# Optimization experiments

Hardware: AMD Instinct MI355X
Metric: run time of the kernel (lower is better)

Reference implementation:

```python
import math
import jax
import jax.numpy as jnp
import numpy as np

MUL = 32            # multiplicity of 0e and 1o in irreps_in/out
N_NODES = 50000
N_EDGES = 800000
N_BASIS = 10
N_HID = 100
NUM_NEIGHBORS = 16.0


def setup_inputs() -> dict:
    key = jax.random.key(0)
    ks = jax.random.split(key, 14)
    return {
        "node_input": jax.random.normal(ks[0], (N_NODES, 4 * MUL), jnp.float32),
        "node_attr": jnp.ones((N_NODES, 1), jnp.float32),
        "edge_src": jax.random.randint(ks[1], (N_EDGES,), 0, N_NODES, dtype=jnp.int32),
        "edge_dst": jax.random.randint(ks[2], (N_EDGES,), 0, N_NODES, dtype=jnp.int32),
        "edge_attr": jax.random.normal(ks[3], (N_EDGES, 4), jnp.float32),
        "edge_length_embedded": jax.random.uniform(ks[4], (N_EDGES, N_BASIS), dtype=jnp.float32),
        "W_sc0": jax.random.normal(ks[5], (MUL, MUL), jnp.float32),
        "W_sc1": jax.random.normal(ks[6], (MUL, MUL), jnp.float32),
        "W_l10": jax.random.normal(ks[7], (MUL, MUL), jnp.float32),
        "W_l11": jax.random.normal(ks[8], (MUL, MUL), jnp.float32),
        "W_l20": jax.random.normal(ks[9], (2 * MUL, MUL), jnp.float32),
        "W_l21": jax.random.normal(ks[10], (2 * MUL, MUL), jnp.float32),
        "W_fc1": jax.random.normal(ks[11], (N_BASIS, N_HID), jnp.float32),
        "W_fc2": jax.random.normal(ks[12], (N_HID, 4 * MUL), jnp.float32),
    }


def _fctp(x0, x1, attr, W0, W1):
    """FullyConnectedTensorProduct with a 1x0e attr: per-irrep linear * scalar attr.
    x0: [N,U], x1: [N,U,3], attr: [N,1]. Path norm alpha = 1/sqrt(fan_in)."""
    inv = 1.0 / math.sqrt(W0.shape[0])
    o0 = attr * (x0 @ W0) * inv                                    # [N,W]
    o1 = attr[:, :, None] * jnp.einsum("nud,uw->nwd", x1, W1) * inv  # [N,W,3]
    return o0, o1


def _forward(node_input, node_attr, edge_attr, edge_length_embedded,
             W_sc0, W_sc1, W_l10, W_l11, W_l20, W_l21, W_fc1, W_fc2,
             edge_src, edge_dst):
    N = node_input.shape[0]
    x0 = node_input[:, :MUL]                       # [N,32]  0e
    x1 = node_input[:, MUL:].reshape(N, MUL, 3)    # [N,32,3] 1o

    # self-connection and lin1 (both attr is scalar 0e)
    s0, s1 = _fctp(x0, x1, node_attr, W_sc0, W_sc1)
    y0, y1 = _fctp(x0, x1, node_attr, W_l10, W_l11)

    # radial MLP -> per-edge uvu weights (weight_numel = 4*MUL)
    h = jax.nn.silu(edge_length_embedded @ W_fc1 * (1.0 / math.sqrt(N_BASIS)))
    w = h @ W_fc2 * (1.0 / math.sqrt(N_HID))       # [E,128]
    w1, w2, w3, w4 = (w[:, 0*MUL:1*MUL], w[:, 1*MUL:2*MUL],
                      w[:, 2*MUL:3*MUL], w[:, 3*MUL:4*MUL])

    # gather source node features per edge
    x0s = y0[edge_src]                              # [E,32]
    x1s = y1[edge_src]                              # [E,32,3]
    ea0 = edge_attr[:, :1]                          # [E,1]   0e
    ea1 = edge_attr[:, 1:]                          # [E,3]   1o

    # segmented uvu tensor product (CG for lmax=1, component norm)
    mid0a = w1 * x0s * ea0                                         # 0e x 0e -> 0e
    mid0b = w4 * jnp.einsum("eum,em->eu", x1s, ea1) * (1.0 / math.sqrt(3.0))  # 1o x 1o -> 0e
    mid1a = (w2 * x0s)[:, :, None] * ea1[:, None, :]               # 0e x 1o -> 1o
    mid1b = w3[:, :, None] * x1s * ea0[:, None, :]                 # 1o x 0e -> 1o
    E = edge_attr.shape[0]
    edge_features = jnp.concatenate(
        [mid0a, mid0b, mid1a.reshape(E, -1), mid1b.reshape(E, -1)], axis=1)  # [E,256]

    # scatter-add to destination nodes
    agg = jax.ops.segment_sum(edge_features, edge_dst, num_segments=N)
    agg = agg * (1.0 / math.sqrt(NUM_NEIGHBORS))

    m0 = agg[:, :2 * MUL]                           # [N,64]  0e part of irreps_mid
    m1 = agg[:, 2 * MUL:].reshape(N, 2 * MUL, 3)    # [N,64,3] 1o part
    z0, z1 = _fctp(m0, m1, node_attr, W_l20, W_l21)

    # sc output_mask is all ones (every output irrep reachable)
    c_s = math.sin(math.pi / 8.0)
    c_x = math.cos(math.pi / 8.0)
    out0 = c_s * s0 + c_x * z0
    out1 = c_s * s1 + c_x * z1
    return jnp.concatenate([out0, out1.reshape(N, -1)], axis=1)   # [N,128]


def reference(node_input, node_attr, edge_src, edge_dst, edge_attr, edge_length_embedded,
              W_sc0, W_sc1, W_l10, W_l11, W_l20, W_l21, W_fc1, W_fc2):
    return _forward(node_input, node_attr, edge_attr, edge_length_embedded,
                    W_sc0, W_sc1, W_l10, W_l11, W_l20, W_l21, W_fc1, W_fc2,
                    edge_src, edge_dst)
```

## Files before the change

### kernel.cpp

```cpp
#include <hip/hip_runtime.h>
#include <hip/hip_bf16.h>

#define MUL 32
#define F4 128
#define NB 10
#define NH 100
#define EROW 136

#define INV_SQRT32 0.17677669529663687f
#define INV_SQRT10 0.31622776601683794f
#define INV_SQRT100 0.1f
#define INV_SQRT3 0.5773502691896258f
#define AGG_SCALE 0.25f
#define INV8 0.125f
#define C_S 0.3826834323650898f
#define C_X 0.9238795325112867f

typedef __attribute__((ext_vector_type(8))) short short8;
typedef __attribute__((ext_vector_type(4))) float float4v;

__device__ __forceinline__ float bf2f(__hip_bfloat16 v) { return __bfloat162float(v); }
__device__ __forceinline__ unsigned short f2b(float x) {
    __hip_bfloat16 b = __float2bfloat16(x);
    return *(unsigned short*)&b;
}
__device__ __forceinline__ float b2f(unsigned short u) {
    __hip_bfloat16 b;
    *(unsigned short*)&b = u;
    return __bfloat162float(b);
}
__device__ __forceinline__ float ldin(const void* p, size_t i, int f) {
    return f ? ((const float*)p)[i] : bf2f(((const __hip_bfloat16*)p)[i]);
}

__global__ void detect_dtype_kernel(const void* __restrict__ node_attr, int* __restrict__ flag) {
    unsigned w = *(const unsigned*)node_attr;
    *flag = (w == 0x3F800000u) ? 1 : 0;
}

__global__ __launch_bounds__(256) void prep_kernel(
    const void* __restrict__ Wfc1,
    const void* __restrict__ Wfc2,
    const void* __restrict__ Wl20,
    const void* __restrict__ Wl21,
    const int* __restrict__ flagp,
    unsigned short* __restrict__ w1t,
    unsigned short* __restrict__ w2t,
    unsigned short* __restrict__ w20t,
    unsigned short* __restrict__ w21t)
{
    int f = *flagp;
    int t = threadIdx.x;
    for (int i = t; i < 128 * 128; i += 256) {
        int n = i >> 7, k = i & 127;
        w2t[i] = (k < NH) ? f2b(ldin(Wfc2, (size_t)k * 128 + n, f)) : 0;
    }
    for (int i = t; i < 32 * 64; i += 256) {
        int v = i >> 6, u = i & 63;
        w20t[i] = f2b(ldin(Wl20, (size_t)u * 32 + v, f));
        w21t[i] = f2b(ldin(Wl21, (size_t)u * 32 + v, f));
    }
    for (int i = t; i < 112 * 32; i += 256) {
        int n = i >> 5, k = i & 31;
        w1t[i] = (k < NB && n < NH) ? f2b(ldin(Wfc1, (size_t)k * NH + n, f)) : 0;
    }
}

__global__ __launch_bounds__(256) void node_y_kernel(
    const void* __restrict__ node_input,
    const void* __restrict__ node_attr,
    const void* __restrict__ Wl10,
    const void* __restrict__ Wl11,
    const int* __restrict__ flagp,
    unsigned short* __restrict__ y, int N)
{
    __shared__ float sW0[1024];
    __shared__ float sW1[1024];
    __shared__ float sX[16 * 128];
    int f = *flagp;
    int t = threadIdx.x;
    for (int i = t; i < 1024; i += 256) {
        sW0[i] = ldin(Wl10, i, f);
        sW1[i] = ldin(Wl11, i, f);
    }
    int n0 = blockIdx.x * 16;
    for (int i = t; i < 2048; i += 256) {
        int ln = i >> 7, c = i & 127, n = n0 + ln;
        sX[i] = (n < N) ? ldin(node_input, (size_t)n * F4 + c, f) : 0.f;
    }
    __syncthreads();
    for (int i = t; i < 2048; i += 256) {
        int ln = i >> 7, c = i & 127, n = n0 + ln;
        if (n >= N) continue;
        float attr = ldin(node_attr, n, f);
        float acc = 0.f;
        if (c < 32) {
#pragma unroll
            for (int u = 0; u < 32; u++) acc += sX[ln * 128 + u] * sW0[u * 32 + c];
        } else {
            int d = (c - 32) >> 5, u0 = (c - 32) & 31;
#pragma unroll
            for (int u = 0; u < 32; u++) acc += sX[ln * 128 + 32 + u * 3 + d] * sW1[u * 32 + u0];
        }
        y[(size_t)n * F4 + c] = f2b(acc * attr * INV_SQRT32);
    }
}

#define SM_ELEB  0
#define SM_HW    4096
#define SM_Y     21504
#define SM_EA    38912
#define SM_SRC   39936
#define SM_DST   40192
#define SM_TOTAL 40448

__global__ __launch_bounds__(256, 4) void fused_edge_kernel(
    const void* __restrict__ ele,
    const void* __restrict__ eattr,
    const int* __restrict__ esrc,
    const int* __restrict__ edst,
    const int* __restrict__ flagp,
    const unsigned short* __restrict__ y,
    const unsigned short* __restrict__ w1t,
    const unsigned short* __restrict__ w2t,
    const unsigned short* __restrict__ w20t,
    const unsigned short* __restrict__ w21t,
    float* __restrict__ agg,
    int E)
{
    __shared__ __align__(16) char smem[SM_TOTAL];
    unsigned short* sEleB = (unsigned short*)(smem + SM_ELEB);
    unsigned short* sHW = (unsigned short*)(smem + SM_HW);
    unsigned short* sY = (unsigned short*)(smem + SM_Y);
    float* sEa = (float*)(smem + SM_EA);
    int* sSrc = (int*)(smem + SM_SRC);
    int* sDst = (int*)(smem + SM_DST);

    int f = *flagp;
    int t = threadIdx.x;
    int e0 = blockIdx.x * 64;
    int ne = E - e0;
    if (ne > 64) ne = 64;

    if (t < 64) {
        sSrc[t] = (t < ne) ? esrc[e0 + t] : 0;
        sDst[t] = (t < ne) ? edst[e0 + t] : 0;
    }
    for (int i = t; i < 64 * 32; i += 256) {
        int e = i >> 5, k = i & 31;
        float v = (k < NB && e < ne) ? ldin(ele, (size_t)(e0 + e) * NB + k, f) : 0.f;
        sEleB[i] = f2b(v);
    }
    {
        int e = t >> 2;
        sEa[t] = (e < ne) ? ldin(eattr, (size_t)e0 * 4 + t, f) : 0.f;
    }
    __syncthreads();

    int w = t >> 6, lane = t & 63;
    int lm = lane & 15, quad = lane >> 4;

    for (int i = t; i < 64 * 16; i += 256) {
        int e = i >> 4, q = i & 15;
        *(uint4*)(sY + e * EROW + q * 8) = *(const uint4*)(y + (size_t)sSrc[e] * 128 + q * 8);
    }

    {
        short8 a = *(const short8*)(sEleB + (w * 16 + lm) * 32 + quad * 8);
        float4v c1[7];
#pragma unroll
        for (int nt = 0; nt < 7; nt++) {
            c1[nt] = (float4v){0.f, 0.f, 0.f, 0.f};
            short8 b = *(const short8*)(w1t + (nt * 16 + lm) * 32 + quad * 8);
            c1[nt] = __builtin_amdgcn_mfma_f32_16x16x32_bf16(a, b, c1[nt], 0, 0, 0);
        }
#pragma unroll
        for (int nt = 0; nt < 7; nt++) {
            int ch = nt * 16 + lm;
#pragma unroll
            for (int r = 0; r < 4; r++) {
                int row = w * 16 + quad * 4 + r;
                float hv = 0.f;
                if (ch < NH) {
                    float aa = c1[nt][r] * INV_SQRT10;
                    hv = aa / (1.f + __expf(-aa));
                }
                sHW[row * EROW + ch] = f2b(hv);
            }
        }
        int e = t >> 2, seg = t & 3;
        *(uint2*)(sHW + e * EROW + 112 + seg * 4) = (uint2){0u, 0u};
    }
    __syncthreads();

    short8 a2[4];
#pragma unroll
    for (int kc = 0; kc < 4; kc++)
        a2[kc] = *(const short8*)(sHW + (w * 16 + lm) * EROW + kc * 32 + quad * 8);
    __syncthreads();
    {
        float4v c2[8];
#pragma unroll
        for (int nt = 0; nt < 8; nt++) c2[nt] = (float4v){0.f, 0.f, 0.f, 0.f};
#pragma unroll
        for (int kc = 0; kc < 4; kc++) {
#pragma unroll
            for (int nt = 0; nt < 8; nt++) {
                short8 b = *(const short8*)(w2t + (nt * 16 + lm) * 128 + kc * 32 + quad * 8);
                c2[nt] = __builtin_amdgcn_mfma_f32_16x16x32_bf16(a2[kc], b, c2[nt], 0, 0, 0);
            }
        }
#pragma unroll
        for (int nt = 0; nt < 8; nt++)
#pragma unroll
            for (int r = 0; r < 4; r++)
                sHW[(w * 16 + quad * 4 + r) * EROW + nt * 16 + lm] = f2b(c2[nt][r] * INV_SQRT100);
    }
    __syncthreads();

    {
        int em = w * 16 + lm;
        const unsigned short* wr = sHW + em * EROW;
        const unsigned short* yr = sY + em * EROW;
        short8 wA = *(const short8*)(wr + quad * 8);
        short8 wB = *(const short8*)(wr + 32 + quad * 8);
        short8 wC = *(const short8*)(wr + 64 + quad * 8);
        short8 wD = *(const short8*)(wr + 96 + quad * 8);
        short8 x0 = *(const short8*)(yr + quad * 8);
        short8 xd0 = *(const short8*)(yr + 32 + quad * 8);
        short8 xd1 = *(const short8*)(yr + 64 + quad * 8);
        short8 xd2 = *(const short8*)(yr + 96 + quad * 8);
        float ea0 = sEa[em * 4 + 0];
        float e1x = sEa[em * 4 + 1];
        float e1y = sEa[em * 4 + 2];
        float e1z = sEa[em * 4 + 3];
        float ea0S = ea0 * AGG_SCALE;
        float s3 = AGG_SCALE * INV_SQRT3;

        short8 f00, f01, f10, f11, f20, f21, f30, f31;
#pragma unroll
        for (int j = 0; j < 8; j++) {
            float x0f = b2f((unsigned short)x0[j]);
            float d0f = b2f((unsigned short)xd0[j]);
            float d1f = b2f((unsigned short)xd1[j]);
            float d2f = b2f((unsigned short)xd2[j]);
            f00[j] = (short)f2b(b2f((unsigned short)wA[j]) * x0f * ea0S);
            float tt = d0f * e1x + d1f * e1y + d2f * e1z;
            f01[j] = (short)f2b(b2f((unsigned short)wD[j]) * tt * s3);
            float p = b2f((unsigned short)wB[j]) * x0f * AGG_SCALE;
            f10[j] = (short)f2b(p * e1x);
            f20[j] = (short)f2b(p * e1y);
            f30[j] = (short)f2b(p * e1z);
            float q = b2f((unsigned short)wC[j]) * ea0S;
            f11[j] = (short)f2b(q * d0f);
            f21[j] = (short)f2b(q * d1f);
            f31[j] = (short)f2b(q * d2f);
        }

        float4v acc[8];
#pragma unroll
        for (int i = 0; i < 8; i++) acc[i] = (float4v){0.f, 0.f, 0.f, 0.f};
#pragma unroll
        for (int g = 0; g < 4; g++) {
            const unsigned short* wt = g ? w21t : w20t;
            short8 ak0 = (g == 0) ? f00 : (g == 1) ? f10 : (g == 2) ? f20 : f30;
            short8 ak1 = (g == 0) ? f01 : (g == 1) ? f11 : (g == 2) ? f21 : f31;
#pragma unroll
            for (int nt = 0; nt < 2; nt++) {
                short8 b0 = *(const short8*)(wt + (nt * 16 + lm) * 64 + quad * 8);
                short8 b1 = *(const short8*)(wt + (nt * 16 + lm) * 64 + 32 + quad * 8);
                acc[g * 2 + nt] = __builtin_amdgcn_mfma_f32_16x16x32_bf16(ak0, b0, acc[g * 2 + nt], 0, 0, 0);
                acc[g * 2 + nt] = __builtin_amdgcn_mfma_f32_16x16x32_bf16(ak1, b1, acc[g * 2 + nt], 0, 0, 0);
            }
        }
#pragma unroll
        for (int g = 0; g < 4; g++)
#pragma unroll
            for (int nt = 0; nt < 2; nt++)
#pragma unroll
                for (int r = 0; r < 4; r++) {
                    int er = w * 16 + quad * 4 + r;
                    if (er < ne) {
                        int ch = (g == 0) ? (nt * 16 + lm) : (32 + (g - 1) * 32 + nt * 16 + lm);
                        atomicAdd(&agg[(size_t)sDst[er] * F4 + ch], acc[g * 2 + nt][r]);
                    }
                }
    }
}

__global__ __launch_bounds__(256) void out_kernel(
    const void* __restrict__ node_input,
    const void* __restrict__ node_attr,
    const void* __restrict__ Wsc0,
    const void* __restrict__ Wsc1,
    const float* __restrict__ agg,
    const int* __restrict__ flagp,
    void* __restrict__ out, int N)
{
    __shared__ float sWs0[1024], sWs1[1024];
    __shared__ float sX[16 * 128];
    __shared__ float sA[16 * 128];
    int f = *flagp;
    int t = threadIdx.x;
    for (int i = t; i < 1024; i += 256) {
        sWs0[i] = ldin(Wsc0, i, f);
        sWs1[i] = ldin(Wsc1, i, f);
    }
    int n0 = blockIdx.x * 16;
    for (int i = t; i < 2048; i += 256) {
        int ln = i >> 7, c = i & 127, n = n0 + ln;
        sX[i] = (n < N) ? ldin(node_input, (size_t)n * F4 + c, f) : 0.f;
        sA[i] = (n < N) ? agg[(size_t)n * F4 + c] : 0.f;
    }
    __syncthreads();
    for (int i = t; i < 2048; i += 256) {
        int ln = i >> 7, c = i & 127, n = n0 + ln;
        if (n >= N) continue;
        float attr = ldin(node_attr, n, f);
        float s, z;
        if (c < 32) {
            float as = 0.f;
#pragma unroll
            for (int u = 0; u < 32; u++) as += sX[ln * 128 + u] * sWs0[u * 32 + c];
            s = as * INV_SQRT32;
            z = sA[ln * 128 + c];
        } else {
            int i2 = c - 32;
            int u0 = i2 / 3, d = i2 - u0 * 3;
            float as = 0.f;
#pragma unroll
            for (int u = 0; u < 32; u++) as += sX[ln * 128 + 32 + u * 3 + d] * sWs1[u * 32 + u0];
            s = as * INV_SQRT32;
            z = sA[ln * 128 + 32 + d * 32 + u0];
        }
        float val = attr * (C_S * s + C_X * z * INV8);
        size_t oi = (size_t)n * F4 + c;
        if (f) ((float*)out)[oi] = val;
        else   ((__hip_bfloat16*)out)[oi] = __float2bfloat16(val);
    }
}

extern "C" void kernel_launch(void* const* d_in, const int* in_sizes, int n_in,
                              void* d_out, int out_size, void* d_ws, size_t ws_size,
                              hipStream_t stream) {
    const void* node_input = d_in[0];
    const void* node_attr  = d_in[1];
    const int* edge_src    = (const int*)d_in[2];
    const int* edge_dst    = (const int*)d_in[3];
    const void* edge_attr  = d_in[4];
    const void* ele        = d_in[5];
    const void* Wsc0       = d_in[6];
    const void* Wsc1       = d_in[7];
    const void* Wl10       = d_in[8];
    const void* Wl11       = d_in[9];
    const void* Wl20       = d_in[10];
    const void* Wl21       = d_in[11];
    const void* Wfc1       = d_in[12];
    const void* Wfc2       = d_in[13];

    int N = in_sizes[0] / F4;
    int E = in_sizes[2];

    char* ws = (char*)d_ws;
    int* flag = (int*)ws;
    unsigned short* y = (unsigned short*)(ws + 64);
    size_t y_b = (size_t)N * F4 * 2;
    float* agg = (float*)(ws + 64 + y_b);
    size_t agg_b = (size_t)N * F4 * 4;
    size_t off = 64 + y_b + agg_b;
    unsigned short* w2t  = (unsigned short*)(ws + off);
    unsigned short* w20t = (unsigned short*)(ws + off + 32768);
    unsigned short* w21t = (unsigned short*)(ws + off + 36864);
    unsigned short* w1t  = (unsigned short*)(ws + off + 40960);

    detect_dtype_kernel<<<1, 1, 0, stream>>>(node_attr, flag);
    prep_kernel<<<1, 256, 0, stream>>>(Wfc1, Wfc2, Wl20, Wl21, flag, w1t, w2t, w20t, w21t);
    hipMemsetAsync(agg, 0, agg_b, stream);

    node_y_kernel<<<(N + 15) / 16, 256, 0, stream>>>(node_input, node_attr, Wl10, Wl11, flag, y, N);

    fused_edge_kernel<<<(E + 63) / 64, 256, 0, stream>>>(
        ele, edge_attr, edge_src, edge_dst, flag, y, w1t, w2t, w20t, w21t, agg, E);

    out_kernel<<<(N + 15) / 16, 256, 0, stream>>>(node_input, node_attr, Wsc0, Wsc1,
                                                  agg, flag, d_out, N);
}
```

Before: 668.7 us.

## Transpose MFMA operands so each edge stays in one lane, drop block syncs

Swaps the MFMA operand roles so edges map to the N dimension. Each lane then owns one edge's row in shared memory, which lets the per-wave shared-memory handoffs replace block-wide __syncthreads. Edge data, src/dst indices and y rows are loaded straight into registers instead of being staged in LDS. Atomic adds now write 4 contiguous channels per lane for one destination node, and the prep kernel is spread over 94 blocks. The cost is more outstanding global loads per thread, and correctness relies on each wave only touching its own rows.

```diff
diff --git a/kernel.cpp b/kernel.cpp
--- a/kernel.cpp
+++ b/kernel.cpp
@@ -50,19 +50,19 @@
     unsigned short* __restrict__ w21t)
 {
     int f = *flagp;
-    int t = threadIdx.x;
-    for (int i = t; i < 128 * 128; i += 256) {
+    int i = blockIdx.x * 256 + threadIdx.x;
+    if (i < 16384) {
         int n = i >> 7, k = i & 127;
         w2t[i] = (k < NH) ? f2b(ldin(Wfc2, (size_t)k * 128 + n, f)) : 0;
-    }
-    for (int i = t; i < 32 * 64; i += 256) {
-        int v = i >> 6, u = i & 63;
-        w20t[i] = f2b(ldin(Wl20, (size_t)u * 32 + v, f));
-        w21t[i] = f2b(ldin(Wl21, (size_t)u * 32 + v, f));
-    }
-    for (int i = t; i < 112 * 32; i += 256) {
-        int n = i >> 5, k = i & 31;
-        w1t[i] = (k < NB && n < NH) ? f2b(ldin(Wfc1, (size_t)k * NH + n, f)) : 0;
+    } else if (i < 18432) {
+        int j = i - 16384; int v = j >> 6, u = j & 63;
+        w20t[j] = f2b(ldin(Wl20, (size_t)u * 32 + v, f));
+    } else if (i < 20480) {
+        int j = i - 18432; int v = j >> 6, u = j & 63;
+        w21t[j] = f2b(ldin(Wl21, (size_t)u * 32 + v, f));
+    } else if (i < 24064) {
+        int j = i - 20480; int n = j >> 5, k = j & 31;
+        w1t[j] = (k < NB && n < NH) ? f2b(ldin(Wfc1, (size_t)k * NH + n, f)) : 0;
     }
 }
 
@@ -106,14 +106,6 @@
     }
 }
 
-#define SM_ELEB  0
-#define SM_HW    4096
-#define SM_Y     21504
-#define SM_EA    38912
-#define SM_SRC   39936
-#define SM_DST   40192
-#define SM_TOTAL 40448
-
 __global__ __launch_bounds__(256, 4) void fused_edge_kernel(
     const void* __restrict__ ele,
     const void* __restrict__ eattr,
@@ -128,76 +120,68 @@
     float* __restrict__ agg,
     int E)
 {
-    __shared__ __align__(16) char smem[SM_TOTAL];
-    unsigned short* sEleB = (unsigned short*)(smem + SM_ELEB);
-    unsigned short* sHW = (unsigned short*)(smem + SM_HW);
-    unsigned short* sY = (unsigned short*)(smem + SM_Y);
-    float* sEa = (float*)(smem + SM_EA);
-    int* sSrc = (int*)(smem + SM_SRC);
-    int* sDst = (int*)(smem + SM_DST);
+    __shared__ __align__(16) unsigned short sHW[64 * EROW];
 
     int f = *flagp;
     int t = threadIdx.x;
-    int e0 = blockIdx.x * 64;
-    int ne = E - e0;
-    if (ne > 64) ne = 64;
-
-    if (t < 64) {
-        sSrc[t] = (t < ne) ? esrc[e0 + t] : 0;
-        sDst[t] = (t < ne) ? edst[e0 + t] : 0;
-    }
-    for (int i = t; i < 64 * 32; i += 256) {
-        int e = i >> 5, k = i & 31;
-        float v = (k < NB && e < ne) ? ldin(ele, (size_t)(e0 + e) * NB + k, f) : 0.f;
-        sEleB[i] = f2b(v);
-    }
+    int w = t >> 6, lane = t & 63, lm = lane & 15, quad = lane >> 4;
+    int e_lm = blockIdx.x * 64 + w * 16 + lm;
+    int e_ld = (e_lm < E) ? e_lm : (E - 1);
+    bool e_ok = (e_lm < E);
+
+    unsigned short* myrow = sHW + (w * 16 + lm) * EROW;
+
+    short8 bE;
+#pragma unroll
+    for (int j = 0; j < 8; j++) {
+        int k = quad * 8 + j;
+        float v = (k < NB) ? ldin(ele, (size_t)e_ld * NB + k, f) : 0.f;
+        bE[j] = (short)f2b(v);
+    }
+    int src = esrc[e_ld];
+    int dst = edst[e_ld];
+    float ea0 = ldin(eattr, (size_t)e_ld * 4 + 0, f);
+    float e1x = ldin(eattr, (size_t)e_ld * 4 + 1, f);
+    float e1y = ldin(eattr, (size_t)e_ld * 4 + 2, f);
+    float e1z = ldin(eattr, (size_t)e_ld * 4 + 3, f);
+    uint4 yq0 = *(const uint4*)(y + (size_t)src * 128 + 0  + quad * 8);
+    uint4 yq1 = *(const uint4*)(y + (size_t)src * 128 + 32 + quad * 8);
+    uint4 yq2 = *(const uint4*)(y + (size_t)src * 128 + 64 + quad * 8);
+    uint4 yq3 = *(const uint4*)(y + (size_t)src * 128 + 96 + quad * 8);
+
     {
-        int e = t >> 2;
-        sEa[t] = (e < ne) ? ldin(eattr, (size_t)e0 * 4 + t, f) : 0.f;
-    }
-    __syncthreads();
-
-    int w = t >> 6, lane = t & 63;
-    int lm = lane & 15, quad = lane >> 4;
-
-    for (int i = t; i < 64 * 16; i += 256) {
-        int e = i >> 4, q = i & 15;
-        *(uint4*)(sY + e * EROW + q * 8) = *(const uint4*)(y + (size_t)sSrc[e] * 128 + q * 8);
-    }
-
-    {
-        short8 a = *(const short8*)(sEleB + (w * 16 + lm) * 32 + quad * 8);
         float4v c1[7];
 #pragma unroll
         for (int nt = 0; nt < 7; nt++) {
             c1[nt] = (float4v){0.f, 0.f, 0.f, 0.f};
-            short8 b = *(const short8*)(w1t + (nt * 16 + lm) * 32 + quad * 8);
-            c1[nt] = __builtin_amdgcn_mfma_f32_16x16x32_bf16(a, b, c1[nt], 0, 0, 0);
+            short8 aW = *(const short8*)(w1t + (nt * 16 + lm) * 32 + quad * 8);
+            c1[nt] = __builtin_amdgcn_mfma_f32_16x16x32_bf16(aW, bE, c1[nt], 0, 0, 0);
         }
 #pragma unroll
         for (int nt = 0; nt < 7; nt++) {
-            int ch = nt * 16 + lm;
+            ushort4 pk;
 #pragma unroll
             for (int r = 0; r < 4; r++) {
-                int row = w * 16 + quad * 4 + r;
+                int ch = nt * 16 + quad * 4 + r;
                 float hv = 0.f;
                 if (ch < NH) {
                     float aa = c1[nt][r] * INV_SQRT10;
                     hv = aa / (1.f + __expf(-aa));
                 }
-                sHW[row * EROW + ch] = f2b(hv);
+                ((unsigned short*)&pk)[r] = f2b(hv);
             }
-        }
-        int e = t >> 2, seg = t & 3;
-        *(uint2*)(sHW + e * EROW + 112 + seg * 4) = (uint2){0u, 0u};
-    }
-    __syncthreads();
-
-    short8 a2[4];
+            *(ushort4*)(myrow + nt * 16 + quad * 4) = pk;
+        }
+        ushort4 z4 = (ushort4){0, 0, 0, 0};
+        *(ushort4*)(myrow + 112 + quad * 4) = z4;
+    }
+    asm volatile("s_waitcnt lgkmcnt(0)" ::: "memory");
+
+    short8 bH[4];
 #pragma unroll
     for (int kc = 0; kc < 4; kc++)
-        a2[kc] = *(const short8*)(sHW + (w * 16 + lm) * EROW + kc * 32 + quad * 8);
-    __syncthreads();
+        bH[kc] = *(const short8*)(myrow + kc * 32 + quad * 8);
+    asm volatile("s_waitcnt lgkmcnt(0)" ::: "memory");
     {
         float4v c2[8];
 #pragma unroll
@@ -206,85 +190,73 @@
         for (int kc = 0; kc < 4; kc++) {
 #pragma unroll
             for (int nt = 0; nt < 8; nt++) {
-                short8 b = *(const short8*)(w2t + (nt * 16 + lm) * 128 + kc * 32 + quad * 8);
-                c2[nt] = __builtin_amdgcn_mfma_f32_16x16x32_bf16(a2[kc], b, c2[nt], 0, 0, 0);
+                short8 aW = *(const short8*)(w2t + (nt * 16 + lm) * 128 + kc * 32 + quad * 8);
+                c2[nt] = __builtin_amdgcn_mfma_f32_16x16x32_bf16(aW, bH[kc], c2[nt], 0, 0, 0);
             }
         }
 #pragma unroll
-        for (int nt = 0; nt < 8; nt++)
+        for (int nt = 0; nt < 8; nt++) {
+            ushort4 pk;
 #pragma unroll
             for (int r = 0; r < 4; r++)
-                sHW[(w * 16 + quad * 4 + r) * EROW + nt * 16 + lm] = f2b(c2[nt][r] * INV_SQRT100);
-    }
-    __syncthreads();
-
-    {
-        int em = w * 16 + lm;
-        const unsigned short* wr = sHW + em * EROW;
-        const unsigned short* yr = sY + em * EROW;
-        short8 wA = *(const short8*)(wr + quad * 8);
-        short8 wB = *(const short8*)(wr + 32 + quad * 8);
-        short8 wC = *(const short8*)(wr + 64 + quad * 8);
-        short8 wD = *(const short8*)(wr + 96 + quad * 8);
-        short8 x0 = *(const short8*)(yr + quad * 8);
-        short8 xd0 = *(const short8*)(yr + 32 + quad * 8);
-        short8 xd1 = *(const short8*)(yr + 64 + quad * 8);
-        short8 xd2 = *(const short8*)(yr + 96 + quad * 8);
-        float ea0 = sEa[em * 4 + 0];
-        float e1x = sEa[em * 4 + 1];
-        float e1y = sEa[em * 4 + 2];
-        float e1z = sEa[em * 4 + 3];
-        float ea0S = ea0 * AGG_SCALE;
-        float s3 = AGG_SCALE * INV_SQRT3;
-
-        short8 f00, f01, f10, f11, f20, f21, f30, f31;
+                ((unsigned short*)&pk)[r] = f2b(c2[nt][r] * INV_SQRT100);
+            *(ushort4*)(myrow + nt * 16 + quad * 4) = pk;
+        }
+    }
+    asm volatile("s_waitcnt lgkmcnt(0)" ::: "memory");
+
+    short8 wv0 = *(const short8*)(myrow + 0  + quad * 8);
+    short8 wv1 = *(const short8*)(myrow + 32 + quad * 8);
+    short8 wv2 = *(const short8*)(myrow + 64 + quad * 8);
+    short8 wv3 = *(const short8*)(myrow + 96 + quad * 8);
+    const unsigned short* y0p = (const unsigned short*)&yq0;
+    const unsigned short* y1p = (const unsigned short*)&yq1;
+    const unsigned short* y2p = (const unsigned short*)&yq2;
+    const unsigned short* y3p = (const unsigned short*)&yq3;
+    float ea0S = ea0 * AGG_SCALE;
+    float s3 = AGG_SCALE * INV_SQRT3;
+
+#pragma unroll
+    for (int g = 0; g < 4; g++) {
+        short8 k0f, k1f;
 #pragma unroll
         for (int j = 0; j < 8; j++) {
-            float x0f = b2f((unsigned short)x0[j]);
-            float d0f = b2f((unsigned short)xd0[j]);
-            float d1f = b2f((unsigned short)xd1[j]);
-            float d2f = b2f((unsigned short)xd2[j]);
-            f00[j] = (short)f2b(b2f((unsigned short)wA[j]) * x0f * ea0S);
-            float tt = d0f * e1x + d1f * e1y + d2f * e1z;
-            f01[j] = (short)f2b(b2f((unsigned short)wD[j]) * tt * s3);
-            float p = b2f((unsigned short)wB[j]) * x0f * AGG_SCALE;
-            f10[j] = (short)f2b(p * e1x);
-            f20[j] = (short)f2b(p * e1y);
-            f30[j] = (short)f2b(p * e1z);
-            float q = b2f((unsigned short)wC[j]) * ea0S;
-            f11[j] = (short)f2b(q * d0f);
-            f21[j] = (short)f2b(q * d1f);
-            f31[j] = (short)f2b(q * d2f);
-        }
-
-        float4v acc[8];
-#pragma unroll
-        for (int i = 0; i < 8; i++) acc[i] = (float4v){0.f, 0.f, 0.f, 0.f};
-#pragma unroll
-        for (int g = 0; g < 4; g++) {
-            const unsigned short* wt = g ? w21t : w20t;
-            short8 ak0 = (g == 0) ? f00 : (g == 1) ? f10 : (g == 2) ? f20 : f30;
-            short8 ak1 = (g == 0) ? f01 : (g == 1) ? f11 : (g == 2) ? f21 : f31;
-#pragma unroll
-            for (int nt = 0; nt < 2; nt++) {
-                short8 b0 = *(const short8*)(wt + (nt * 16 + lm) * 64 + quad * 8);
-                short8 b1 = *(const short8*)(wt + (nt * 16 + lm) * 64 + 32 + quad * 8);
-                acc[g * 2 + nt] = __builtin_amdgcn_mfma_f32_16x16x32_bf16(ak0, b0, acc[g * 2 + nt], 0, 0, 0);
-                acc[g * 2 + nt] = __builtin_amdgcn_mfma_f32_16x16x32_bf16(ak1, b1, acc[g * 2 + nt], 0, 0, 0);
+            float x0f = b2f(y0p[j]);
+            float d0f = b2f(y1p[j]);
+            float d1f = b2f(y2p[j]);
+            float d2f = b2f(y3p[j]);
+            float w1v = b2f((unsigned short)wv0[j]);
+            float w2v = b2f((unsigned short)wv1[j]);
+            float w3v = b2f((unsigned short)wv2[j]);
+            float w4v = b2f((unsigned short)wv3[j]);
+            float k0, k1;
+            if (g == 0) {
+                k0 = w1v * x0f * ea0S;
+                k1 = w4v * (d0f * e1x + d1f * e1y + d2f * e1z) * s3;
+            } else {
+                float ed = (g == 1) ? e1x : (g == 2) ? e1y : e1z;
+                float dd = (g == 1) ? d0f : (g == 2) ? d1f : d2f;
+                k0 = w2v * x0f * AGG_SCALE * ed;
+                k1 = w3v * dd * ea0S;
             }
-        }
-#pragma unroll
-        for (int g = 0; g < 4; g++)
-#pragma unroll
-            for (int nt = 0; nt < 2; nt++)
-#pragma unroll
-                for (int r = 0; r < 4; r++) {
-                    int er = w * 16 + quad * 4 + r;
-                    if (er < ne) {
-                        int ch = (g == 0) ? (nt * 16 + lm) : (32 + (g - 1) * 32 + nt * 16 + lm);
-                        atomicAdd(&agg[(size_t)sDst[er] * F4 + ch], acc[g * 2 + nt][r]);
-                    }
-                }
+            k0f[j] = (short)f2b(k0);
+            k1f[j] = (short)f2b(k1);
+        }
+        const unsigned short* wt = g ? w21t : w20t;
+        int chbase = (g == 0) ? 0 : 32 + (g - 1) * 32;
+#pragma unroll
+        for (int nt = 0; nt < 2; nt++) {
+            float4v acc = (float4v){0.f, 0.f, 0.f, 0.f};
+            short8 a0 = *(const short8*)(wt + (nt * 16 + lm) * 64 + 0  + quad * 8);
+            short8 a1 = *(const short8*)(wt + (nt * 16 + lm) * 64 + 32 + quad * 8);
+            acc = __builtin_amdgcn_mfma_f32_16x16x32_bf16(a0, k0f, acc, 0, 0, 0);
+            acc = __builtin_amdgcn_mfma_f32_16x16x32_bf16(a1, k1f, acc, 0, 0, 0);
+            if (e_ok) {
+                float* base = agg + (size_t)dst * F4 + chbase + nt * 16 + quad * 4;
+#pragma unroll
+                for (int r = 0; r < 4; r++) atomicAdd(base + r, acc[r]);
+            }
+        }
     }
 }
 
@@ -374,7 +346,7 @@
     unsigned short* w1t  = (unsigned short*)(ws + off + 40960);
 
     detect_dtype_kernel<<<1, 1, 0, stream>>>(node_attr, flag);
-    prep_kernel<<<1, 256, 0, stream>>>(Wfc1, Wfc2, Wl20, Wl21, flag, w1t, w2t, w20t, w21t);
+    prep_kernel<<<94, 256, 0, stream>>>(Wfc1, Wfc2, Wl20, Wl21, flag, w1t, w2t, w20t, w21t);
     hipMemsetAsync(agg, 0, agg_b, stream);
 
     node_y_kernel<<<(N + 15) / 16, 256, 0, stream>>>(node_input, node_attr, Wl10, Wl11, flag, y, N);
```

Result: slower. 1.559 ms (+133.2%).
